# Performance work log

Hardware: AMD Instinct MI355X
Metric: run time of the kernel (lower is better)

The kernel has to match this reference:

```python
import jax, jax.numpy as jnp
import numpy as np

NUM_HEADS = 12


def setup_inputs() -> dict:
    key = jax.random.key(0)
    ks = jax.random.split(key, 6)
    B, H, W, C = 8, 32, 32, 768
    hd = C // NUM_HEADS
    n = lambda k, shp, sc: jax.random.normal(k, shp, dtype=jnp.float32) * sc
    return {
        "x": n(ks[0], (B, H, W, C), 1.0),
        "qkv_w": n(ks[1], (3 * C, C), 0.02),
        "qkv_b": jnp.zeros((3 * C,), jnp.float32),
        "proj_w": n(ks[2], (C, C), 0.02),
        "proj_b": jnp.zeros((C,), jnp.float32),
        "rel_pos_h": n(ks[3], (2 * H - 1, hd), 0.02),
        "rel_pos_w": n(ks[4], (2 * W - 1, hd), 0.02),
    }


def reference(x, qkv_w, qkv_b, proj_w, proj_b, rel_pos_h, rel_pos_w):
    B, H, W, C = x.shape
    nH = NUM_HEADS
    hd = C // nH
    scale = hd ** -0.5
    # qkv projection (torch Linear convention: y = x @ W.T + b)
    qkv = x.reshape(B, H * W, C) @ qkv_w.T + qkv_b              # (B, HW, 3C)
    qkv = qkv.reshape(B, H * W, 3, nH, hd).transpose(2, 0, 3, 1, 4)
    qkv = qkv.reshape(3, B * nH, H * W, hd)
    q, k, v = qkv[0], qkv[1], qkv[2]
    attn = jnp.einsum('bqd,bkd->bqk', q * scale, k)             # (B*nH, HW, HW)
    # decomposed relative position bias (q_size == k_size, so no interpolation)
    coords_h = jnp.arange(H)[:, None] - jnp.arange(H)[None, :] + (H - 1)
    coords_w = jnp.arange(W)[:, None] - jnp.arange(W)[None, :] + (W - 1)
    Rh = rel_pos_h[coords_h]                                    # (H, H, hd)
    Rw = rel_pos_w[coords_w]                                    # (W, W, hd)
    r_q = q.reshape(B * nH, H, W, hd)
    rel_h = jnp.einsum('bhwc,hkc->bhwk', r_q, Rh)               # (B*nH, H, W, H)
    rel_w = jnp.einsum('bhwc,wkc->bhwk', r_q, Rw)               # (B*nH, H, W, W)
    attn = (attn.reshape(B * nH, H, W, H, W)
            + rel_h[..., :, None] + rel_w[..., None, :]).reshape(B * nH, H * W, H * W)
    attn = jax.nn.softmax(attn, axis=-1)
    out = attn @ v                                              # (B*nH, HW, hd)
    out = out.reshape(B, nH, H, W, hd).transpose(0, 2, 3, 1, 4).reshape(B, H, W, C)
    return out @ proj_w.T + proj_b
```

## Files before the change

kernel.cpp:

```cpp
#include <hip/hip_runtime.h>

using u16 = unsigned short;
using u32 = unsigned int;
typedef __attribute__((ext_vector_type(8))) short bf16x8;
typedef __attribute__((ext_vector_type(4))) float f32x4;

__device__ __forceinline__ float bf2f(u32 h) {
  union { u32 u; float f; } c; c.u = h << 16; return c.f;
}
__device__ __forceinline__ u16 f2bf(float f) {
  union { float f; u32 u; } c; c.f = f;
  u32 u = c.u;
  u32 r = (u + 0x7FFFu + ((u >> 16) & 1u)) >> 16;
  return (u16)r;
}

#define GLD16(gsrc, ldst)                                                      \
  __builtin_amdgcn_global_load_lds(                                            \
      (const __attribute__((address_space(1))) unsigned int*)(gsrc),           \
      (__attribute__((address_space(3))) unsigned int*)(ldst), 16, 0, 0)

__device__ __forceinline__ int kappa(int ss) {
  return (ss & 0x23) | ((ss & 0x10) >> 2) | ((ss & 0x0C) << 1);
}

__device__ __forceinline__ bf16x8 onehot8(int c) {
  union { u32 w[4]; bf16x8 v; } u;
  u32 hv = (c & 1) ? 0x3F800000u : 0x3F80u;
#pragma unroll
  for (int k = 0; k < 4; ++k) u.w[k] = ((c >> 1) == k) ? hv : 0u;
  return u.v;
}

__global__ void prep_kernel(const float* __restrict__ x, const float* __restrict__ qw,
                            const float* __restrict__ pw, const float* __restrict__ rph,
                            const float* __restrict__ rpw, u16* __restrict__ xb,
                            u16* __restrict__ qwb, u16* __restrict__ pwb,
                            u16* __restrict__ tbl) {
  int i = blockIdx.x * 256 + threadIdx.x;
  const float* src;
  u16* dst;
  int j;
  if (i < 1572864) { src = x; dst = xb; j = i; }
  else if (i < 2015232) { src = qw; dst = qwb; j = i - 1572864; }
  else if (i < 2162688) { src = pw; dst = pwb; j = i - 2015232; }
  else {
    int b = (i - 2162688) * 4;
    ushort4 o;
#pragma unroll
    for (int k = 0; k < 4; ++k) {
      int idx = b + k, row = idx >> 6, d = idx & 63;
      float v = 0.f;
      if (row < 63) v = rph[row * 64 + d];
      else if (row >= 64 && row < 127) v = rpw[(row - 64) * 64 + d];
      ((u16*)&o)[k] = f2bf(v * 8.0f);
    }
    *(ushort4*)&tbl[b] = o;
    return;
  }
  float4 v = *(const float4*)(src + j * 4);
  ushort4 o;
  o.x = f2bf(v.x); o.y = f2bf(v.y); o.z = f2bf(v.z); o.w = f2bf(v.w);
  *(ushort4*)(dst + j * 4) = o;
}

__global__ __launch_bounds__(256, 2) void pgemm_kernel(
    const u16* __restrict__ A, const u16* __restrict__ tbl, u16* __restrict__ Q2) {
  __shared__ u16 As[2][128 * 64];
  __shared__ u16 Bs[128 * 64];
  const int tid = threadIdx.x;
  const int lane = tid & 63, wave = tid >> 6;
  const int lr = lane & 15, lg = lane >> 4;
  const int m0 = blockIdx.x * 256;
  const int wm = (wave >> 1) * 64, wn = (wave & 1) * 64;

#pragma unroll
  for (int i = 0; i < 4; ++i) {
    int c = tid + i * 256;
    int row = c >> 3, pp = c & 7;
    int pl = pp ^ (row & 7);
    GLD16(tbl + row * 64 + pl * 8, &Bs[c * 8]);
#pragma unroll
    for (int tt = 0; tt < 2; ++tt)
      GLD16(A + (size_t)(m0 + tt * 128 + row) * 128 + pl * 8, &As[tt][c * 8]);
  }
  __syncthreads();

  bf16x8 b[4][2];
#pragma unroll
  for (int n = 0; n < 4; ++n) {
    int row = wn + n * 16 + lr;
#pragma unroll
    for (int kf = 0; kf < 2; ++kf)
      b[n][kf] = *(const bf16x8*)&Bs[(row * 64 + kf * 32 + lg * 8) ^ ((row & 7) << 3)];
  }

#pragma unroll
  for (int tt = 0; tt < 2; ++tt) {
    bf16x8 a[4][2];
#pragma unroll
    for (int m = 0; m < 4; ++m) {
      int row = wm + m * 16 + lr;
#pragma unroll
      for (int kf = 0; kf < 2; ++kf)
        a[m][kf] = *(const bf16x8*)&As[tt][(row * 64 + kf * 32 + lg * 8) ^ ((row & 7) << 3)];
    }
    f32x4 acc[4][4] = {};
#pragma unroll
    for (int kf = 0; kf < 2; ++kf)
#pragma unroll
      for (int m = 0; m < 4; ++m)
#pragma unroll
        for (int n = 0; n < 4; ++n)
          acc[m][n] = __builtin_amdgcn_mfma_f32_16x16x32_bf16(a[m][kf], b[n][kf], acc[m][n], 0, 0, 0);

#pragma unroll
    for (int m = 0; m < 4; ++m)
#pragma unroll
      for (int n = 0; n < 4; ++n) {
        const int col = wn + n * 16 + lr;
#pragma unroll
        for (int r = 0; r < 4; ++r) {
          const int g = m0 + tt * 128 + wm + m * 16 + lg * 4 + r;
          const int s = g & 1023;
          const int hq = s >> 5, w = s & 31;
          u16 hv = f2bf(acc[m][n][r]);
          if (col < 64) {
            int kh = hq + 31 - col;
            if ((unsigned)kh < 32u) Q2[(size_t)g * 128 + 96 + kh] = hv;
          } else {
            int kw = w + 95 - col;
            if ((unsigned)kw < 32u) Q2[(size_t)g * 128 + 64 + kw] = hv;
          }
        }
      }
  }
}

template <int MODE>
__global__ __launch_bounds__(512, 2) void gemm128(
    const u16* __restrict__ A, const u16* __restrict__ B,
    const float* __restrict__ bias, u16* __restrict__ oq, u16* __restrict__ ok,
    u16* __restrict__ ovt, float* __restrict__ ofp) {
  __shared__ u16 As[2][128 * 64];
  __shared__ u16 Bs[2][128 * 64];
  const int tid = threadIdx.x;
  const int lane = tid & 63, wave = tid >> 6;
  const int lr = lane & 15, lg = lane >> 4;

  const int nbx = (MODE == 0) ? 18 : 6;
  const int nwg = nbx * 64;
  int id = blockIdx.y * nbx + blockIdx.x;
  int nid = (id & 7) * (nwg >> 3) + (id >> 3);
  const int m0 = (nid / nbx) * 128, n0 = (nid % nbx) * 128;
  const int wm = (wave >> 2) * 64, wn = (wave & 3) * 32;

  f32x4 acc[4][2] = {};

  int aoff[4][2], boff[2][2];
#pragma unroll
  for (int m = 0; m < 4; ++m) {
    int row = wm + m * 16 + lr;
#pragma unroll
    for (int kf = 0; kf < 2; ++kf)
      aoff[m][kf] = (row * 64 + kf * 32 + lg * 8) ^ ((row & 7) << 3);
  }
#pragma unroll
  for (int n = 0; n < 2; ++n) {
    int row = wn + n * 16 + lr;
#pragma unroll
    for (int kf = 0; kf < 2; ++kf)
      boff[n][kf] = (row * 64 + kf * 32 + lg * 8) ^ ((row & 7) << 3);
  }

  const u16* ap[2];
  const u16* bp[2];
#pragma unroll
  for (int i = 0; i < 2; ++i) {
    int c = tid + i * 512;
    int row = c >> 3, pp = c & 7;
    int pl = pp ^ (row & 7);
    if constexpr (MODE == 0) {
      ap[i] = A + (size_t)(m0 + row) * 768 + pl * 8;
    } else {
      int g = m0 + row;
      ap[i] = A + ((size_t)((g >> 10) * 12) << 16) + (g & 1023) * 64 + pl * 8;
    }
    bp[i] = B + (size_t)(n0 + row) * 768 + pl * 8;
  }
  constexpr int dA = (MODE == 0) ? 64 : 65536;

  auto stage = [&](int bi) {
#pragma unroll
    for (int i = 0; i < 2; ++i) {
      int c = tid + i * 512;
      GLD16(ap[i], &As[bi][c * 8]);
      GLD16(bp[i], &Bs[bi][c * 8]);
      ap[i] += dA;
      bp[i] += 64;
    }
  };

  stage(0);
#pragma unroll 1
  for (int t = 0; t < 12; ++t) {
    const int cur = t & 1;
    if (t < 11) {
      stage(cur ^ 1);
      asm volatile("s_waitcnt vmcnt(4)" ::: "memory");
    } else {
      asm volatile("s_waitcnt vmcnt(0)" ::: "memory");
    }
    __builtin_amdgcn_sched_barrier(0);
    __builtin_amdgcn_s_barrier();
    __builtin_amdgcn_sched_barrier(0);

    bf16x8 a[4][2], b[2][2];
#pragma unroll
    for (int m = 0; m < 4; ++m)
#pragma unroll
      for (int kf = 0; kf < 2; ++kf)
        a[m][kf] = *(const bf16x8*)&As[cur][aoff[m][kf]];
#pragma unroll
    for (int n = 0; n < 2; ++n)
#pragma unroll
      for (int kf = 0; kf < 2; ++kf)
        b[n][kf] = *(const bf16x8*)&Bs[cur][boff[n][kf]];
    __builtin_amdgcn_s_setprio(1);
#pragma unroll
    for (int kf = 0; kf < 2; ++kf)
#pragma unroll
      for (int m = 0; m < 4; ++m)
#pragma unroll
        for (int n = 0; n < 2; ++n)
          acc[m][n] = __builtin_amdgcn_mfma_f32_16x16x32_bf16(a[m][kf], b[n][kf], acc[m][n], 0, 0, 0);
    __builtin_amdgcn_s_setprio(0);

    __builtin_amdgcn_sched_barrier(0);
    __builtin_amdgcn_s_barrier();
    __builtin_amdgcn_sched_barrier(0);
  }

#pragma unroll
  for (int m = 0; m < 4; ++m) {
    const int grow0 = m0 + wm + m * 16 + lg * 4;
#pragma unroll
    for (int n = 0; n < 2; ++n) {
      const int gcol = n0 + wn + n * 16 + lr;
      const float bv = bias[gcol];
      if constexpr (MODE == 0) {
        int which = (gcol >= 1536) ? 2 : (gcol >= 768 ? 1 : 0);
        int rem = gcol - which * 768;
        int bh = (grow0 >> 10) * 12 + (rem >> 6);
        if (which == 2) {
          int s0 = grow0 & 1023;
          int colb = (s0 & ~63) | kappa(s0 & 63);
          ushort4 pk;
          pk.x = f2bf(acc[m][n][0] + bv);
          pk.y = f2bf(acc[m][n][1] + bv);
          pk.z = f2bf(acc[m][n][2] + bv);
          pk.w = f2bf(acc[m][n][3] + bv);
          *(ushort4*)&ovt[((size_t)bh << 16) + (size_t)(rem & 63) * 1024 + colb] = pk;
        } else if (which == 0) {
#pragma unroll
          for (int r = 0; r < 4; ++r) {
            int s = (grow0 & 1023) + r;
            oq[((size_t)bh << 17) + s * 128 + (rem & 63)] =
                f2bf((acc[m][n][r] + bv) * 0.18033688f);
          }
        } else {
#pragma unroll
          for (int r = 0; r < 4; ++r) {
            int s = (grow0 & 1023) + r;
            ok[((size_t)bh << 16) + s * 64 + (rem & 63)] = f2bf(acc[m][n][r] + bv);
          }
        }
      } else {
#pragma unroll
        for (int r = 0; r < 4; ++r)
          ofp[(size_t)(grow0 + r) * 768 + gcol] = acc[m][n][r] + bv;
      }
    }
  }
}

__global__ __launch_bounds__(256, 2) void attn_kernel(
    const u16* __restrict__ qb, const u16* __restrict__ kb,
    const u16* __restrict__ vtb, u16* __restrict__ ao) {
  __shared__ u16 Ks[2][4096];
  __shared__ u16 Vs[2][4096];

  const int tid = threadIdx.x;
  const int lane = tid & 63, wave = tid >> 6;
  const int lr = lane & 15, lg = lane >> 4;
  const int bh = blockIdx.x;
  const int q0 = blockIdx.y * 128 + wave * 32;
  const size_t hb2 = (size_t)bh << 17;
  const size_t hbv = (size_t)bh << 16;

  bf16x8 qf[2][4];
#pragma unroll
  for (int m = 0; m < 2; ++m)
#pragma unroll
    for (int kf = 0; kf < 4; ++kf)
      qf[m][kf] = *(const bf16x8*)(qb + hb2 + (size_t)(q0 + m * 16 + lr) * 128 + kf * 32 + lg * 8);

  f32x4 sacW[2][2] = {};
#pragma unroll
  for (int h = 0; h < 2; ++h) {
    bf16x8 kwf = onehot8(h * 16 + lr - lg * 8);
#pragma unroll
    for (int m = 0; m < 2; ++m)
      sacW[m][h] = __builtin_amdgcn_mfma_f32_16x16x32_bf16(kwf, qf[m][2], sacW[m][h], 0, 0, 0);
  }

  float lsum[2] = {};
  f32x4 acco[2][4] = {};

  const u16* kp[2];
  const u16* vp[2];
#pragma unroll
  for (int i = 0; i < 2; ++i) {
    int c = tid + i * 256;
    int row = c >> 3, pp = c & 7;
    int pl = pp ^ (row & 7);
    kp[i] = kb + hbv + (size_t)row * 64 + pl * 8;
    vp[i] = vtb + hbv + (size_t)row * 1024 + pl * 8;
  }

  auto stage = [&](int bi) {
#pragma unroll
    for (int i = 0; i < 2; ++i) {
      int c = tid + i * 256;
      GLD16(kp[i], &Ks[bi][c * 8]);
      GLD16(vp[i], &Vs[bi][c * 8]);
      kp[i] += 4096;
      vp[i] += 64;
    }
  };

  stage(0);

#pragma unroll 1
  for (int t = 0; t < 16; ++t) {
    const int cur = t & 1;
    if (t < 15) {
      stage(cur ^ 1);
      asm volatile("s_waitcnt vmcnt(4)" ::: "memory");
    } else {
      asm volatile("s_waitcnt vmcnt(0)" ::: "memory");
    }
    __builtin_amdgcn_sched_barrier(0);
    __builtin_amdgcn_s_barrier();
    __builtin_amdgcn_sched_barrier(0);

    bf16x8 khf[2];
#pragma unroll
    for (int h = 0; h < 2; ++h) khf[h] = onehot8(2 * t + h - lg * 8);

    f32x4 sac[2][4];
#pragma unroll
    for (int m = 0; m < 2; ++m)
#pragma unroll
      for (int f = 0; f < 4; ++f) sac[m][f] = sacW[m][f & 1];
    __builtin_amdgcn_s_setprio(1);
#pragma unroll
    for (int kf = 0; kf < 2; ++kf) {
#pragma unroll
      for (int f = 0; f < 4; ++f) {
        int row = f * 16 + lr;
        bf16x8 kv = *(const bf16x8*)&Ks[cur][(row * 64 + kf * 32 + lg * 8) ^ ((row & 7) << 3)];
#pragma unroll
        for (int m = 0; m < 2; ++m)
          sac[m][f] = __builtin_amdgcn_mfma_f32_16x16x32_bf16(kv, qf[m][kf], sac[m][f], 0, 0, 0);
      }
    }
#pragma unroll
    for (int f = 0; f < 4; ++f)
#pragma unroll
      for (int m = 0; m < 2; ++m)
        sac[m][f] = __builtin_amdgcn_mfma_f32_16x16x32_bf16(khf[f >> 1], qf[m][3], sac[m][f], 0, 0, 0);
    __builtin_amdgcn_s_setprio(0);

    bf16x8 paf[2][2];
#pragma unroll
    for (int m = 0; m < 2; ++m) {
      union { u32 w[4]; bf16x8 v; } wa, wb;
#pragma unroll
      for (int f = 0; f < 4; ++f) {
        float p0 = __builtin_amdgcn_exp2f(sac[m][f][0]);
        float p1 = __builtin_amdgcn_exp2f(sac[m][f][1]);
        float p2 = __builtin_amdgcn_exp2f(sac[m][f][2]);
        float p3 = __builtin_amdgcn_exp2f(sac[m][f][3]);
        lsum[m] += (p0 + p1) + (p2 + p3);
        u32 w0, w1;
        asm("v_cvt_pk_bf16_f32 %0, %1, %2" : "=v"(w0) : "v"(p0), "v"(p1));
        asm("v_cvt_pk_bf16_f32 %0, %1, %2" : "=v"(w1) : "v"(p2), "v"(p3));
        if (f < 2) { wa.w[f * 2] = w0; wa.w[f * 2 + 1] = w1; }
        else       { wb.w[(f - 2) * 2] = w0; wb.w[(f - 2) * 2 + 1] = w1; }
      }
      paf[m][0] = wa.v;
      paf[m][1] = wb.v;
    }

    __builtin_amdgcn_s_setprio(1);
#pragma unroll
    for (int kf = 0; kf < 2; ++kf) {
#pragma unroll
      for (int fd = 0; fd < 4; ++fd) {
        int drow = fd * 16 + lr;
        bf16x8 vv = *(const bf16x8*)&Vs[cur][(drow * 64 + kf * 32 + lg * 8) ^ ((drow & 7) << 3)];
#pragma unroll
        for (int m = 0; m < 2; ++m)
          acco[m][fd] = __builtin_amdgcn_mfma_f32_16x16x32_bf16(paf[m][kf], vv, acco[m][fd], 0, 0, 0);
      }
    }
    __builtin_amdgcn_s_setprio(0);

    __builtin_amdgcn_sched_barrier(0);
    __builtin_amdgcn_s_barrier();
    __builtin_amdgcn_sched_barrier(0);
  }

#pragma unroll
  for (int m = 0; m < 2; ++m) {
    float s = lsum[m];
    s += __shfl_xor(s, 16);
    s += __shfl_xor(s, 32);
    float inv = 1.0f / s;
#pragma unroll
    for (int r = 0; r < 4; ++r) {
      int src = (lane & 48) + ((lane & 48) >> 2) + r;
      float invr = __shfl(inv, src);
      int gq = q0 + m * 16 + lg * 4 + r;
#pragma unroll
      for (int fd = 0; fd < 4; ++fd)
        ao[hbv + (size_t)gq * 64 + fd * 16 + lr] = f2bf(acco[m][fd][r] * invr);
    }
  }
}

extern "C" void kernel_launch(void* const* d_in, const int* in_sizes, int n_in,
                              void* d_out, int out_size, void* d_ws, size_t ws_size,
                              hipStream_t stream) {
  const float* x = (const float*)d_in[0];
  const float* qkv_w = (const float*)d_in[1];
  const float* qkv_b = (const float*)d_in[2];
  const float* proj_w = (const float*)d_in[3];
  const float* proj_b = (const float*)d_in[4];
  const float* rel_pos_h = (const float*)d_in[5];
  const float* rel_pos_w = (const float*)d_in[6];
  float* out = (float*)d_out;

  char* ws = (char*)d_ws;
  u16* x_bf = (u16*)(ws + 0);
  u16* qkvw_bf = (u16*)(ws + 12582912);
  u16* projw_bf = (u16*)(ws + 16121856);
  u16* qbuf2 = (u16*)(ws + 17301504);
  u16* kbuf = (u16*)(ws + 42467328);
  u16* vtbuf = (u16*)(ws + 55050240);
  u16* tbl = (u16*)(ws + 67633152);
  u16* aobuf = x_bf;

  prep_kernel<<<8456, 256, 0, stream>>>(x, qkv_w, proj_w, rel_pos_h, rel_pos_w,
                                        x_bf, qkvw_bf, projw_bf, tbl);

  gemm128<0><<<dim3(18, 64), 512, 0, stream>>>(x_bf, qkvw_bf, qkv_b, qbuf2, kbuf, vtbuf, nullptr);

  pgemm_kernel<<<384, 256, 0, stream>>>(qbuf2, tbl, qbuf2);

  attn_kernel<<<dim3(96, 8), 256, 0, stream>>>(qbuf2, kbuf, vtbuf, aobuf);

  gemm128<1><<<dim3(6, 64), 512, 0, stream>>>(aobuf, projw_bf, proj_b, nullptr, nullptr, nullptr, out);
}
```

Measured before the change: 120.5 us.

## Switch GEMM to 256x128 tiles with K=32 stages and 2x4 wave layout

```diff
diff --git a/kernel.cpp b/kernel.cpp
--- a/kernel.cpp
+++ b/kernel.cpp
@@ -138,76 +138,74 @@
 }
 
 template <int MODE>
-__global__ __launch_bounds__(512, 2) void gemm128(
+__global__ __launch_bounds__(512, 4) void gemm128(
     const u16* __restrict__ A, const u16* __restrict__ B,
     const float* __restrict__ bias, u16* __restrict__ oq, u16* __restrict__ ok,
     u16* __restrict__ ovt, float* __restrict__ ofp) {
-  __shared__ u16 As[2][128 * 64];
-  __shared__ u16 Bs[2][128 * 64];
+  __shared__ u16 As[2][256 * 32];
+  __shared__ u16 Bs[2][128 * 32];
   const int tid = threadIdx.x;
   const int lane = tid & 63, wave = tid >> 6;
   const int lr = lane & 15, lg = lane >> 4;
 
   const int nbx = (MODE == 0) ? 18 : 6;
-  const int nwg = nbx * 64;
+  const int nwg = nbx * 32;
   int id = blockIdx.y * nbx + blockIdx.x;
   int nid = (id & 7) * (nwg >> 3) + (id >> 3);
-  const int m0 = (nid / nbx) * 128, n0 = (nid % nbx) * 128;
-  const int wm = (wave >> 2) * 64, wn = (wave & 3) * 32;
-
-  f32x4 acc[4][2] = {};
-
-  int aoff[4][2], boff[2][2];
+  const int m0 = (nid / nbx) * 256, n0 = (nid % nbx) * 128;
+  const int wm = (wave >> 1) * 64, wn = (wave & 1) * 64;
+
+  f32x4 acc[4][4] = {};
+
+  int aoff[4], boff[4];
 #pragma unroll
   for (int m = 0; m < 4; ++m) {
     int row = wm + m * 16 + lr;
-#pragma unroll
-    for (int kf = 0; kf < 2; ++kf)
-      aoff[m][kf] = (row * 64 + kf * 32 + lg * 8) ^ ((row & 7) << 3);
-  }
-#pragma unroll
-  for (int n = 0; n < 2; ++n) {
+    aoff[m] = row * 32 + ((lg ^ (row & 3)) * 8);
+  }
+#pragma unroll
+  for (int n = 0; n < 4; ++n) {
     int row = wn + n * 16 + lr;
-#pragma unroll
-    for (int kf = 0; kf < 2; ++kf)
-      boff[n][kf] = (row * 64 + kf * 32 + lg * 8) ^ ((row & 7) << 3);
+    boff[n] = row * 32 + ((lg ^ (row & 3)) * 8);
   }
 
   const u16* ap[2];
-  const u16* bp[2];
+  const u16* bp;
 #pragma unroll
   for (int i = 0; i < 2; ++i) {
     int c = tid + i * 512;
-    int row = c >> 3, pp = c & 7;
-    int pl = pp ^ (row & 7);
+    int row = c >> 2, pp = c & 3;
+    int pl = pp ^ (row & 3);
     if constexpr (MODE == 0) {
       ap[i] = A + (size_t)(m0 + row) * 768 + pl * 8;
     } else {
       int g = m0 + row;
       ap[i] = A + ((size_t)((g >> 10) * 12) << 16) + (g & 1023) * 64 + pl * 8;
     }
-    bp[i] = B + (size_t)(n0 + row) * 768 + pl * 8;
-  }
-  constexpr int dA = (MODE == 0) ? 64 : 65536;
-
-  auto stage = [&](int bi) {
-#pragma unroll
-    for (int i = 0; i < 2; ++i) {
-      int c = tid + i * 512;
-      GLD16(ap[i], &As[bi][c * 8]);
-      GLD16(bp[i], &Bs[bi][c * 8]);
-      ap[i] += dA;
-      bp[i] += 64;
-    }
+  }
+  {
+    int row = tid >> 2, pp = tid & 3;
+    int pl = pp ^ (row & 3);
+    bp = B + (size_t)(n0 + row) * 768 + pl * 8;
+  }
+
+  auto stage = [&](int bi, int advA) {
+    GLD16(ap[0], &As[bi][tid * 8]);
+    GLD16(ap[1], &As[bi][(tid + 512) * 8]);
+    GLD16(bp, &Bs[bi][tid * 8]);
+    ap[0] += advA;
+    ap[1] += advA;
+    bp += 32;
   };
 
-  stage(0);
+  stage(0, 32);
 #pragma unroll 1
-  for (int t = 0; t < 12; ++t) {
+  for (int t = 0; t < 24; ++t) {
     const int cur = t & 1;
-    if (t < 11) {
-      stage(cur ^ 1);
-      asm volatile("s_waitcnt vmcnt(4)" ::: "memory");
+    if (t < 23) {
+      int advA = (MODE == 1) ? ((((t + 1) & 1)) ? 65504 : 32) : 32;
+      stage(cur ^ 1, advA);
+      asm volatile("s_waitcnt vmcnt(3)" ::: "memory");
     } else {
       asm volatile("s_waitcnt vmcnt(0)" ::: "memory");
     }
@@ -215,25 +213,17 @@
     __builtin_amdgcn_s_barrier();
     __builtin_amdgcn_sched_barrier(0);
 
-    bf16x8 a[4][2], b[2][2];
+    bf16x8 a[4], b[4];
+#pragma unroll
+    for (int m = 0; m < 4; ++m) a[m] = *(const bf16x8*)&As[cur][aoff[m]];
+#pragma unroll
+    for (int n = 0; n < 4; ++n) b[n] = *(const bf16x8*)&Bs[cur][boff[n]];
+    __builtin_amdgcn_s_setprio(1);
 #pragma unroll
     for (int m = 0; m < 4; ++m)
 #pragma unroll
-      for (int kf = 0; kf < 2; ++kf)
-        a[m][kf] = *(const bf16x8*)&As[cur][aoff[m][kf]];
-#pragma unroll
-    for (int n = 0; n < 2; ++n)
-#pragma unroll
-      for (int kf = 0; kf < 2; ++kf)
-        b[n][kf] = *(const bf16x8*)&Bs[cur][boff[n][kf]];
-    __builtin_amdgcn_s_setprio(1);
-#pragma unroll
-    for (int kf = 0; kf < 2; ++kf)
-#pragma unroll
-      for (int m = 0; m < 4; ++m)
-#pragma unroll
-        for (int n = 0; n < 2; ++n)
-          acc[m][n] = __builtin_amdgcn_mfma_f32_16x16x32_bf16(a[m][kf], b[n][kf], acc[m][n], 0, 0, 0);
+      for (int n = 0; n < 4; ++n)
+        acc[m][n] = __builtin_amdgcn_mfma_f32_16x16x32_bf16(a[m], b[n], acc[m][n], 0, 0, 0);
     __builtin_amdgcn_s_setprio(0);
 
     __builtin_amdgcn_sched_barrier(0);
@@ -245,7 +235,7 @@
   for (int m = 0; m < 4; ++m) {
     const int grow0 = m0 + wm + m * 16 + lg * 4;
 #pragma unroll
-    for (int n = 0; n < 2; ++n) {
+    for (int n = 0; n < 4; ++n) {
       const int gcol = n0 + wn + n * 16 + lr;
       const float bv = bias[gcol];
       if constexpr (MODE == 0) {
@@ -465,11 +455,11 @@
   prep_kernel<<<8456, 256, 0, stream>>>(x, qkv_w, proj_w, rel_pos_h, rel_pos_w,
                                         x_bf, qkvw_bf, projw_bf, tbl);
 
-  gemm128<0><<<dim3(18, 64), 512, 0, stream>>>(x_bf, qkvw_bf, qkv_b, qbuf2, kbuf, vtbuf, nullptr);
+  gemm128<0><<<dim3(18, 32), 512, 0, stream>>>(x_bf, qkvw_bf, qkv_b, qbuf2, kbuf, vtbuf, nullptr);
 
   pgemm_kernel<<<384, 256, 0, stream>>>(qbuf2, tbl, qbuf2);
 
   attn_kernel<<<dim3(96, 8), 256, 0, stream>>>(qbuf2, kbuf, vtbuf, aobuf);
 
-  gemm128<1><<<dim3(6, 64), 512, 0, stream>>>(aobuf, projw_bf, proj_b, nullptr, nullptr, nullptr, out);
-}
+  gemm128<1><<<dim3(6, 32), 512, 0, stream>>>(aobuf, projw_bf, proj_b, nullptr, nullptr, nullptr, out);
+}
```

Result: slower. 136.3 us (+13.1%).
